# Performance work log

Measured on AMD Instinct MI355X. Metric: run time of the kernel, lower is better.

Reference implementation:

```python
import jax, jax.numpy as jnp
import numpy as np

R = 3          # routing iterations (init arg r)
EPS = 1e-7     # init arg epsilon


def squash(s, axis=-1):
    # squash(s) = ||s||^2 / (1 + ||s||^2) * s / (||s|| + EPS)
    n = jnp.linalg.norm(s, axis=axis, keepdims=True)
    n2 = jnp.square(n)
    return (n2 / (1.0 + n2)) * (s / (n + EPS))


def setup_inputs() -> dict:
    key = jax.random.key(0)
    k1, k2 = jax.random.split(key)
    B, S, P, J, I = 32, 32, 2048, 32, 16
    inputs = jax.random.normal(k1, (B, P, I), dtype=jnp.float32)
    # tf.random_normal_initializer default stddev = 0.05
    W = jax.random.normal(k2, (S, P, J, I), dtype=jnp.float32) * 0.05
    return {"inputs": inputs, "W": W}


def reference(inputs, W):
    # u_hat[b,s,p,j] = sum_i W[s,p,j,i] * inputs[b,p,i]
    u_hat = jnp.einsum('spji,bpi->bspj', W, inputs)  # [B,S,P,J]
    B, S, P, J = u_hat.shape
    b = jnp.zeros((B, S, 1, P), dtype=u_hat.dtype)
    v = None
    for _ in range(R):
        c = jax.nn.softmax(b, axis=-1)                     # over primary caps
        s = jnp.einsum('bsxp,bspj->bsxj', c, u_hat)        # [B,S,1,J]
        v = squash(s)                                      # [B,S,1,J]
        agreement = jnp.einsum('bsxj,bspj->bsxp', v, u_hat)  # [B,S,1,P]
        b = b + agreement
    return v.reshape(B, S, J)
```

## Files before the change

### kernel.cpp

```cpp
#include <hip/hip_runtime.h>
#include <stdint.h>

#define B_ 32
#define S_ 32
#define P_ 2048
#define J_ 32
#define I_ 16

#define PLSTRIDE ((size_t)S_ * P_ * 32)

typedef _Float16 half8_t __attribute__((ext_vector_type(8)));
typedef float f32x16 __attribute__((ext_vector_type(16)));

__device__ inline float f16lo(uint32_t d) {
    return (float)__builtin_bit_cast(_Float16, (unsigned short)(d & 0xffffu));
}
__device__ inline float f16hi(uint32_t d) {
    return (float)__builtin_bit_cast(_Float16, (unsigned short)(d >> 16));
}

__global__ __launch_bounds__(256) void uhat_kernel(
        const float* __restrict__ W, const float* __restrict__ X,
        uint32_t* __restrict__ U) {
    const int tid  = threadIdx.x;
    const int lane = tid & 63;
    const int wave = tid >> 6;
    const int l31  = lane & 31;
    const int lhi  = lane >> 5;
    const int s    = blockIdx.y;
    const int p0   = blockIdx.x * 16 + wave * 4;

    float4 wv[4][2], xv[4][2];
    #pragma unroll
    for (int t = 0; t < 4; ++t) {
        const int p = p0 + t;
        const float* wr = W + (((size_t)s * P_ + p) * J_ + l31) * I_ + lhi * 8;
        wv[t][0] = *reinterpret_cast<const float4*>(wr);
        wv[t][1] = *reinterpret_cast<const float4*>(wr + 4);
        const float* xr = X + ((size_t)l31 * P_ + p) * I_ + lhi * 8;
        xv[t][0] = *reinterpret_cast<const float4*>(xr);
        xv[t][1] = *reinterpret_cast<const float4*>(xr + 4);
    }

    #pragma unroll
    for (int t = 0; t < 4; ++t) {
        const int p = p0 + t;
        half8_t A, Bf;
        A[0] = (_Float16)xv[t][0].x; A[1] = (_Float16)xv[t][0].y;
        A[2] = (_Float16)xv[t][0].z; A[3] = (_Float16)xv[t][0].w;
        A[4] = (_Float16)xv[t][1].x; A[5] = (_Float16)xv[t][1].y;
        A[6] = (_Float16)xv[t][1].z; A[7] = (_Float16)xv[t][1].w;
        Bf[0] = (_Float16)wv[t][0].x; Bf[1] = (_Float16)wv[t][0].y;
        Bf[2] = (_Float16)wv[t][0].z; Bf[3] = (_Float16)wv[t][0].w;
        Bf[4] = (_Float16)wv[t][1].x; Bf[5] = (_Float16)wv[t][1].y;
        Bf[6] = (_Float16)wv[t][1].z; Bf[7] = (_Float16)wv[t][1].w;

        f32x16 acc = {};
        acc = __builtin_amdgcn_mfma_f32_32x32x16_f16(A, Bf, acc, 0, 0, 0);

        const size_t rowbase = ((size_t)s * P_ + p) * 32 + l31;
        #pragma unroll
        for (int m = 0; m < 8; ++m) {
            uint32_t lo = (uint32_t)__builtin_bit_cast(
                unsigned short, (_Float16)acc[2 * m]);
            uint32_t hi = (uint32_t)__builtin_bit_cast(
                unsigned short, (_Float16)acc[2 * m + 1]);
            const int plane = (m << 1) | lhi;
            U[(size_t)plane * PLSTRIDE + rowbase] = lo | (hi << 16);
        }
    }
}

template <int MASK, int HALF>
__device__ inline void red_level(float* red, int lane) {
    const bool hi = (lane & MASK) != 0;
    #pragma unroll
    for (int k = 0; k < HALF; ++k) {
        float send = hi ? red[k] : red[k + HALF];
        float recv = __shfl_xor(send, MASK, 64);
        red[k] = (hi ? red[k + HALF] : red[k]) + recv;
    }
}

__global__ __launch_bounds__(1024) void routing_kernel(
        const uint32_t* __restrict__ U, float* __restrict__ out) {
    const int tid  = threadIdx.x;
    const int lane = tid & 63;
    const int wid  = tid >> 6;

    const int hw   = blockIdx.x;
    const int L    = (hw & 7) * 128 + (hw >> 3);
    const int par  = L & 1;
    const int pairIdx = L >> 1;
    const int plane = pairIdx >> 5;
    const int s     = pairIdx & 31;
    const int m     = plane >> 1;
    const int lhi   = plane & 1;
    const int b     = ((2 * m) & 3) + 8 * (m >> 1) + 4 * lhi + par;

    __shared__ float sred[16 * 32];
    __shared__ float vlds[32];
    __shared__ float scal[32];

    const uint4* ub4 = reinterpret_cast<const uint4*>(
        U + (size_t)plane * PLSTRIDE + ((size_t)s * P_ + 2 * (size_t)tid) * 32);
    uint32_t a[32];
    #pragma unroll
    for (int c = 0; c < 4; ++c) {
        uint4 q0 = ub4[c * 4 + 0];
        uint4 q1 = ub4[c * 4 + 1];
        uint4 q2 = ub4[c * 4 + 2];
        uint4 q3 = ub4[c * 4 + 3];
        uint32_t D[16] = {q0.x, q0.y, q0.z, q0.w, q1.x, q1.y, q1.z, q1.w,
                          q2.x, q2.y, q2.z, q2.w, q3.x, q3.y, q3.z, q3.w};
        if (par == 0) {
            #pragma unroll
            for (int k = 0; k < 8; ++k)
                a[c * 8 + k] = (D[2 * k] & 0xffffu) | (D[2 * k + 1] << 16);
        } else {
            #pragma unroll
            for (int k = 0; k < 8; ++k)
                a[c * 8 + k] = (D[2 * k] >> 16) | (D[2 * k + 1] & 0xffff0000u);
        }
        __builtin_amdgcn_sched_barrier(0);
    }

    float bp0 = 0.0f, bp1 = 0.0f;

    for (int it = 0; it < 3; ++it) {
        float c0, c1;
        if (it == 0) {
            c0 = c1 = 1.0f / 2048.0f;
        } else {
            float mx = fmaxf(bp0, bp1);
            #pragma unroll
            for (int msk = 32; msk >= 1; msk >>= 1)
                mx = fmaxf(mx, __shfl_xor(mx, msk, 64));
            if (lane == 0) scal[wid] = mx;
            __syncthreads();
            mx = scal[0];
            #pragma unroll
            for (int w2 = 1; w2 < 16; ++w2) mx = fmaxf(mx, scal[w2]);
            float e0 = __expf(bp0 - mx);
            float e1 = __expf(bp1 - mx);
            float zs = e0 + e1;
            #pragma unroll
            for (int msk = 32; msk >= 1; msk >>= 1)
                zs += __shfl_xor(zs, msk, 64);
            if (lane == 0) scal[16 + wid] = zs;
            __syncthreads();
            float Z = 0.0f;
            #pragma unroll
            for (int w2 = 0; w2 < 16; ++w2) Z += scal[16 + w2];
            float invZ = 1.0f / Z;
            c0 = e0 * invZ;
            c1 = e1 * invZ;
        }

        float red[32];
        #pragma unroll
        for (int k = 0; k < 16; ++k) {
            uint32_t d0 = a[k], d1 = a[16 + k];
            red[2 * k]     = fmaf(c0, f16lo(d0), c1 * f16lo(d1));
            red[2 * k + 1] = fmaf(c0, f16hi(d0), c1 * f16hi(d1));
        }
        red_level<32, 16>(red, lane);
        red_level<16, 8>(red, lane);
        red_level<8, 4>(red, lane);
        red_level<4, 2>(red, lane);
        red_level<2, 1>(red, lane);
        red[0] += __shfl_xor(red[0], 1, 64);
        if ((lane & 1) == 0) sred[wid * 32 + (lane >> 1)] = red[0];
        __syncthreads();

        if (tid < 32) {
            float sv = 0.0f;
            #pragma unroll
            for (int w2 = 0; w2 < 16; ++w2) sv += sred[w2 * 32 + tid];
            float sq = sv * sv;
            #pragma unroll
            for (int msk = 16; msk >= 1; msk >>= 1)
                sq += __shfl_xor(sq, msk, 64);
            float n = sqrtf(sq);
            float scale = sq / ((1.0f + sq) * (n + 1e-7f));
            float v = sv * scale;
            vlds[tid] = v;
            if (it == 2) out[((size_t)b * S_ + s) * J_ + tid] = v;
        }
        __syncthreads();

        if (it < 2) {
            const float2* vl2 = reinterpret_cast<const float2*>(vlds);
            float ag0 = 0.0f, ag1 = 0.0f;
            #pragma unroll
            for (int k = 0; k < 16; ++k) {
                float2 vk = vl2[k];
                uint32_t d0 = a[k], d1 = a[16 + k];
                ag0 = fmaf(vk.x, f16lo(d0), ag0);
                ag0 = fmaf(vk.y, f16hi(d0), ag0);
                ag1 = fmaf(vk.x, f16lo(d1), ag1);
                ag1 = fmaf(vk.y, f16hi(d1), ag1);
            }
            bp0 += ag0;
            bp1 += ag1;
        }
    }
}

extern "C" void kernel_launch(void* const* d_in, const int* in_sizes, int n_in,
                              void* d_out, int out_size, void* d_ws, size_t ws_size,
                              hipStream_t stream) {
    (void)in_sizes; (void)n_in; (void)out_size;
    const float* X = (const float*)d_in[0];
    const float* W = (const float*)d_in[1];
    float* out     = (float*)d_out;
    uint32_t* U    = (uint32_t*)d_ws;

    const size_t need = (size_t)B_ * S_ * P_ * J_ * 2;
    if (ws_size < need) return;

    dim3 g1(P_ / 16, S_);
    uhat_kernel<<<g1, 256, 0, stream>>>(W, X, U);
    routing_kernel<<<16 * S_ * 2, 1024, 0, stream>>>(U, out);
}
```

Baseline: 122.4 us.

## Store u_hat per batch contiguously with lane-shuffle packing and nontemporal access

```diff
diff --git a/kernel.cpp b/kernel.cpp
--- a/kernel.cpp
+++ b/kernel.cpp
@@ -7,10 +7,12 @@
 #define J_ 32
 #define I_ 16
 
-#define PLSTRIDE ((size_t)S_ * P_ * 32)
+#define UROW 16
+#define UBSTRIDE ((size_t)S_ * P_ * UROW)
 
 typedef _Float16 half8_t __attribute__((ext_vector_type(8)));
 typedef float f32x16 __attribute__((ext_vector_type(16)));
+typedef uint32_t u32x4 __attribute__((ext_vector_type(4)));
 
 __device__ inline float f16lo(uint32_t d) {
     return (float)__builtin_bit_cast(_Float16, (unsigned short)(d & 0xffffu));
@@ -27,6 +29,7 @@
     const int wave = tid >> 6;
     const int l31  = lane & 31;
     const int lhi  = lane >> 5;
+    const int lpar = lane & 1;
     const int s    = blockIdx.y;
     const int p0   = blockIdx.x * 16 + wave * 4;
 
@@ -58,15 +61,20 @@
         f32x16 acc = {};
         acc = __builtin_amdgcn_mfma_f32_32x32x16_f16(A, Bf, acc, 0, 0, 0);
 
-        const size_t rowbase = ((size_t)s * P_ + p) * 32 + l31;
+        const size_t rowbase = ((size_t)s * P_ + p) * UROW + (l31 >> 1);
         #pragma unroll
-        for (int m = 0; m < 8; ++m) {
-            uint32_t lo = (uint32_t)__builtin_bit_cast(
-                unsigned short, (_Float16)acc[2 * m]);
-            uint32_t hi = (uint32_t)__builtin_bit_cast(
-                unsigned short, (_Float16)acc[2 * m + 1]);
-            const int plane = (m << 1) | lhi;
-            U[(size_t)plane * PLSTRIDE + rowbase] = lo | (hi << 16);
+        for (int rp = 0; rp < 8; ++rp) {
+            const int r = 2 * rp;
+            uint32_t lo16 = (uint32_t)__builtin_bit_cast(
+                unsigned short, (_Float16)acc[r]);
+            uint32_t hi16 = (uint32_t)__builtin_bit_cast(
+                unsigned short, (_Float16)acc[r + 1]);
+            uint32_t hp = lo16 | (hi16 << 16);
+            uint32_t tp = (uint32_t)__shfl_xor((int)hp, 1, 64);
+            uint32_t d = lpar ? ((tp >> 16) | (hp & 0xffff0000u))
+                              : ((hp & 0xffffu) | (tp << 16));
+            const int b = (r & 3) + lpar + 8 * (r >> 2) + 4 * lhi;
+            __builtin_nontemporal_store(d, &U[(size_t)b * UBSTRIDE + rowbase]);
         }
     }
 }
@@ -87,42 +95,20 @@
     const int tid  = threadIdx.x;
     const int lane = tid & 63;
     const int wid  = tid >> 6;
-
-    const int hw   = blockIdx.x;
-    const int L    = (hw & 7) * 128 + (hw >> 3);
-    const int par  = L & 1;
-    const int pairIdx = L >> 1;
-    const int plane = pairIdx >> 5;
-    const int s     = pairIdx & 31;
-    const int m     = plane >> 1;
-    const int lhi   = plane & 1;
-    const int b     = ((2 * m) & 3) + 8 * (m >> 1) + 4 * lhi + par;
+    const int bs   = blockIdx.x;
 
     __shared__ float sred[16 * 32];
     __shared__ float vlds[32];
     __shared__ float scal[32];
 
-    const uint4* ub4 = reinterpret_cast<const uint4*>(
-        U + (size_t)plane * PLSTRIDE + ((size_t)s * P_ + 2 * (size_t)tid) * 32);
+    const u32x4* ub = reinterpret_cast<const u32x4*>(
+        U + (size_t)bs * ((size_t)P_ * UROW) + (size_t)tid * 32);
     uint32_t a[32];
     #pragma unroll
-    for (int c = 0; c < 4; ++c) {
-        uint4 q0 = ub4[c * 4 + 0];
-        uint4 q1 = ub4[c * 4 + 1];
-        uint4 q2 = ub4[c * 4 + 2];
-        uint4 q3 = ub4[c * 4 + 3];
-        uint32_t D[16] = {q0.x, q0.y, q0.z, q0.w, q1.x, q1.y, q1.z, q1.w,
-                          q2.x, q2.y, q2.z, q2.w, q3.x, q3.y, q3.z, q3.w};
-        if (par == 0) {
-            #pragma unroll
-            for (int k = 0; k < 8; ++k)
-                a[c * 8 + k] = (D[2 * k] & 0xffffu) | (D[2 * k + 1] << 16);
-        } else {
-            #pragma unroll
-            for (int k = 0; k < 8; ++k)
-                a[c * 8 + k] = (D[2 * k] >> 16) | (D[2 * k + 1] & 0xffff0000u);
-        }
-        __builtin_amdgcn_sched_barrier(0);
+    for (int k = 0; k < 8; ++k) {
+        u32x4 t = __builtin_nontemporal_load(&ub[k]);
+        a[k * 4 + 0] = t[0]; a[k * 4 + 1] = t[1];
+        a[k * 4 + 2] = t[2]; a[k * 4 + 3] = t[3];
     }
 
     float bp0 = 0.0f, bp1 = 0.0f;
@@ -185,7 +171,7 @@
             float scale = sq / ((1.0f + sq) * (n + 1e-7f));
             float v = sv * scale;
             vlds[tid] = v;
-            if (it == 2) out[((size_t)b * S_ + s) * J_ + tid] = v;
+            if (it == 2) out[(size_t)bs * J_ + tid] = v;
         }
         __syncthreads();
 
@@ -221,5 +207,5 @@
 
     dim3 g1(P_ / 16, S_);
     uhat_kernel<<<g1, 256, 0, stream>>>(W, X, U);
-    routing_kernel<<<16 * S_ * 2, 1024, 0, stream>>>(U, out);
-}
+    routing_kernel<<<B_ * S_, 1024, 0, stream>>>(U, out);
+}
```

New measurement: 134.6 us. +10.0%, slower.
